# Kernel tuning notes

Hardware: AMD Instinct MI355X
Metric: run time of the kernel (lower is better)

## Reference

```python
import jax, jax.numpy as jnp
import numpy as np

N_NODES = 8192
N_EDGES = 262144
IN_DIM = 128
HID = 128
FLAT = N_NODES * HID  # 1048576


def gcn_conv(x, edge_index, W, b):
    """PyG-style GCNConv: add self-loops, symmetric deg^{-1/2} normalization,
    out[col] += norm * (x @ W)[row], plus bias."""
    N = x.shape[0]
    loop = jnp.arange(N)
    row = jnp.concatenate([edge_index[0], loop])  # source nodes
    col = jnp.concatenate([edge_index[1], loop])  # target nodes
    deg = jax.ops.segment_sum(jnp.ones_like(col, dtype=x.dtype), col, num_segments=N)
    dinv = jax.lax.rsqrt(jnp.maximum(deg, 1.0))  # deg >= 1 thanks to self-loops
    norm = dinv[row] * dinv[col]  # [E+N]
    h = x @ W  # [N, out]
    msg = h[row] * norm[:, None]  # gather
    out = jax.ops.segment_sum(msg, col, num_segments=N)  # scatter-add
    return out + b


def setup_inputs() -> dict:
    key = jax.random.key(0)
    ks = jax.random.split(key, 12)
    def lin(k, fan_in, shape):
        bound = 1.0 / np.sqrt(fan_in)
        return jax.random.uniform(k, shape, jnp.float32, -bound, bound)
    return {
        "x": jax.random.normal(ks[0], (N_NODES, IN_DIM), jnp.float32),
        "edge_index": jax.random.randint(ks[1], (2, N_EDGES), 0, N_NODES, jnp.int64 if jax.config.jax_enable_x64 else jnp.int32),
        "W1": lin(ks[2], IN_DIM, (IN_DIM, HID)),
        "b1": lin(ks[3], IN_DIM, (HID,)),
        "W2": lin(ks[4], HID, (HID, HID)),
        "b2": lin(ks[5], HID, (HID,)),
        "fc1_w": lin(ks[6], FLAT, (FLAT, HID)),
        "fc1_b": lin(ks[7], FLAT, (HID,)),
        "fc2_w": lin(ks[8], HID, (HID, HID)),
        "fc2_b": lin(ks[9], HID, (HID,)),
        "fc3_w": lin(ks[10], HID, (HID, 1)),
        "fc3_b": lin(ks[11], HID, (1,)),
    }


def reference(x, edge_index, W1, b1, W2, b2, fc1_w, fc1_b, fc2_w, fc2_b, fc3_w, fc3_b):
    e = jax.nn.relu(gcn_conv(x, edge_index, W1, b1))
    e = gcn_conv(e, edge_index, W2, b2)
    flat = e.reshape(-1)  # [N_NODES*HID]
    h = jax.nn.relu(flat @ fc1_w + fc1_b)
    h = jax.nn.relu(h @ fc2_w + fc2_b)
    q = h @ fc3_w + fc3_b  # [1]
    return q
```

## Files before the change

### kernel.cpp

```cpp
#include <hip/hip_runtime.h>

#define N_NODES 8192
#define N_EDGES 262144
#define DIM 128
#define NREP 64

typedef float fv4 __attribute__((ext_vector_type(4)));

__global__ void k_deg(const int* __restrict__ col, int* __restrict__ deg) {
    int e = blockIdx.x * blockDim.x + threadIdx.x;
    if (e < N_EDGES) atomicAdd(&deg[col[e]], 1);
}

__global__ __launch_bounds__(1024) void k_scan(const int* __restrict__ deg,
                                               int* __restrict__ rowptr,
                                               float* __restrict__ dinv) {
    __shared__ int wsum[16];
    __shared__ int wpre[16];
    int t = threadIdx.x;
    int base = t * 8;
    int v[8];
    int s = 0;
    #pragma unroll
    for (int i = 0; i < 8; ++i) {
        int d = deg[base + i];
        dinv[base + i] = rsqrtf((float)d + 1.0f);
        v[i] = s; s += d;
    }
    int lane = t & 63, wv = t >> 6;
    int incl = s;
    #pragma unroll
    for (int off = 1; off < 64; off <<= 1) {
        int n = __shfl_up(incl, off);
        if (lane >= off) incl += n;
    }
    if (lane == 63) wsum[wv] = incl;
    __syncthreads();
    if (t == 0) {
        int a = 0;
        #pragma unroll
        for (int i = 0; i < 16; ++i) { wpre[i] = a; a += wsum[i]; }
        rowptr[8192] = a;
    }
    __syncthreads();
    int ebase = wpre[wv] + incl - s;
    #pragma unroll
    for (int i = 0; i < 8; ++i) rowptr[base + i] = ebase + v[i];
}

__global__ void k_fill(const int* __restrict__ rows, const int* __restrict__ cols,
                       const int* __restrict__ rowptr, int* __restrict__ cnt,
                       int* __restrict__ srcs) {
    int e = blockIdx.x * blockDim.x + threadIdx.x;
    if (e < N_EDGES) {
        int c = cols[e];
        int p = atomicAdd(&cnt[c], 1);
        srcs[rowptr[c] + p] = rows[e];
    }
}

__global__ __launch_bounds__(256) void k_gemm(const float* __restrict__ x,
                                              const float* __restrict__ W,
                                              const float* __restrict__ dinv,
                                              float* __restrict__ out) {
    __shared__ float4 Wl[128 * 32];
    int t = threadIdx.x;
    const float4* W4 = (const float4*)W;
    for (int i = t; i < 128 * 32; i += 256) Wl[i] = W4[i];
    __syncthreads();

    int q  = t & 31;
    int rg = t >> 5;
    int row0 = blockIdx.x * 32;
    for (int p = 0; p < 4; ++p) {
        int row = row0 + p * 8 + rg;
        const float4* xr = (const float4*)(x + (size_t)row * DIM);
        float4 acc = {0.f, 0.f, 0.f, 0.f};
        #pragma unroll
        for (int k4 = 0; k4 < 32; ++k4) {
            float4 xv = xr[k4];
            float4 w0 = Wl[(k4 * 4 + 0) * 32 + q];
            float4 w1 = Wl[(k4 * 4 + 1) * 32 + q];
            float4 w2 = Wl[(k4 * 4 + 2) * 32 + q];
            float4 w3 = Wl[(k4 * 4 + 3) * 32 + q];
            acc.x += xv.x * w0.x + xv.y * w1.x + xv.z * w2.x + xv.w * w3.x;
            acc.y += xv.x * w0.y + xv.y * w1.y + xv.z * w2.y + xv.w * w3.y;
            acc.z += xv.x * w0.z + xv.y * w1.z + xv.z * w2.z + xv.w * w3.z;
            acc.w += xv.x * w0.w + xv.y * w1.w + xv.z * w2.w + xv.w * w3.w;
        }
        float s = dinv[row];
        acc.x *= s; acc.y *= s; acc.z *= s; acc.w *= s;
        ((float4*)(out + (size_t)row * DIM))[q] = acc;
    }
}

__device__ __forceinline__ float2 gather_row(const float2* __restrict__ H,
                                             const int* __restrict__ srcs,
                                             int beg, int end, int node, int lane) {
    float2 a0 = H[(size_t)node * 64 + lane];
    float2 a1 = {0.f, 0.f};
    int j = beg;
    int npre = (4 - (beg & 3)) & 3;
    if (npre > end - beg) npre = end - beg;
    for (int p = 0; p < npre; ++p, ++j) {
        float2 v = H[(size_t)srcs[j] * 64 + lane];
        a0.x += v.x; a0.y += v.y;
    }
    for (; j + 3 < end; j += 4) {
        int4 s4 = *reinterpret_cast<const int4*>(srcs + j);
        float2 v0 = H[(size_t)s4.x * 64 + lane];
        float2 v1 = H[(size_t)s4.y * 64 + lane];
        float2 v2 = H[(size_t)s4.z * 64 + lane];
        float2 v3 = H[(size_t)s4.w * 64 + lane];
        a0.x += v0.x + v2.x; a0.y += v0.y + v2.y;
        a1.x += v1.x + v3.x; a1.y += v1.y + v3.y;
    }
    for (; j < end; ++j) {
        float2 v = H[(size_t)srcs[j] * 64 + lane];
        a1.x += v.x; a1.y += v.y;
    }
    a0.x += a1.x; a0.y += a1.y;
    return a0;
}

__global__ __launch_bounds__(256) void k_gather(const float* __restrict__ h,
                                                const int* __restrict__ srcs,
                                                const int* __restrict__ rowptr,
                                                const float* __restrict__ dinv,
                                                const float* __restrict__ b,
                                                float* __restrict__ out) {
    int t = threadIdx.x;
    int lane = t & 63;
    int node = blockIdx.x * 4 + (t >> 6);
    float2 acc = gather_row((const float2*)h, srcs, rowptr[node], rowptr[node + 1], node, lane);
    float s = dinv[node];
    float2 bv = ((const float2*)b)[lane];
    float2 o;
    o.x = fmaxf(s * acc.x + bv.x, 0.f);
    o.y = fmaxf(s * acc.y + bv.y, 0.f);
    ((float2*)(out + (size_t)node * DIM))[lane] = o;
}

__global__ __launch_bounds__(256) void k_gfc(const float* __restrict__ h,
                                             const int* __restrict__ srcs,
                                             const int* __restrict__ rowptr,
                                             const float* __restrict__ dinv,
                                             const float* __restrict__ b,
                                             const float* __restrict__ w,
                                             float* __restrict__ facc_r) {
    __shared__ float oL[4][128];
    __shared__ fv4 red4[4][32];
    int t = threadIdx.x;
    int lane = t & 63;
    int wid = t >> 6;
    int node = blockIdx.x * 4 + wid;
    float2 acc = gather_row((const float2*)h, srcs, rowptr[node], rowptr[node + 1], node, lane);
    float s = dinv[node];
    float2 bv = ((const float2*)b)[lane];
    float2 o = { s * acc.x + bv.x, s * acc.y + bv.y };
    ((float2*)oL[wid])[lane] = o;
    __syncthreads();

    int q  = lane & 31;
    int kh = lane >> 5;
    size_t rowbase = (size_t)node * 128;
    fv4 a4 = {0.f, 0.f, 0.f, 0.f};
    #pragma unroll 8
    for (int k2 = 0; k2 < 64; ++k2) {
        int k = k2 * 2 + kh;
        float ok = oL[wid][k];
        const fv4* wp = (const fv4*)(w + (rowbase + k) * 128);
        fv4 wr = __builtin_nontemporal_load(wp + q);
        a4 += ok * wr;
    }
    a4.x += __shfl_xor(a4.x, 32);
    a4.y += __shfl_xor(a4.y, 32);
    a4.z += __shfl_xor(a4.z, 32);
    a4.w += __shfl_xor(a4.w, 32);
    if (lane < 32) red4[wid][q] = a4;
    __syncthreads();
    if (t < 128) {
        const float* rf = (const float*)red4;
        float val = (rf[t] + rf[128 + t]) + (rf[256 + t] + rf[384 + t]);
        atomicAdd(&facc_r[((blockIdx.x & (NREP - 1)) << 7) + t], val);
    }
}

__global__ __launch_bounds__(128) void k_tail(const float* __restrict__ facc_r,
                                              const float* __restrict__ fc1_b,
                                              const float* __restrict__ fc2_w,
                                              const float* __restrict__ fc2_b,
                                              const float* __restrict__ fc3_w,
                                              const float* __restrict__ fc3_b,
                                              float* __restrict__ out) {
    __shared__ float h1[128], red[128];
    int j = threadIdx.x;
    float a0 = 0.f;
    #pragma unroll
    for (int r = 0; r < NREP; ++r) a0 += facc_r[r * 128 + j];
    h1[j] = fmaxf(a0 + fc1_b[j], 0.f);
    __syncthreads();
    float a = 0.f;
    #pragma unroll 8
    for (int k = 0; k < 128; ++k) a += h1[k] * fc2_w[k * 128 + j];
    float h2 = fmaxf(a + fc2_b[j], 0.f);
    red[j] = h2 * fc3_w[j];
    __syncthreads();
    if (j == 0) {
        float s = 0.f;
        for (int k = 0; k < 128; ++k) s += red[k];
        out[0] = s + fc3_b[0];
    }
}

extern "C" void kernel_launch(void* const* d_in, const int* in_sizes, int n_in,
                              void* d_out, int out_size, void* d_ws, size_t ws_size,
                              hipStream_t stream) {
    const float* x     = (const float*)d_in[0];
    const int*   ei    = (const int*)d_in[1];
    const float* W1    = (const float*)d_in[2];
    const float* b1    = (const float*)d_in[3];
    const float* W2    = (const float*)d_in[4];
    const float* b2    = (const float*)d_in[5];
    const float* fc1_w = (const float*)d_in[6];
    const float* fc1_b = (const float*)d_in[7];
    const float* fc2_w = (const float*)d_in[8];
    const float* fc2_b = (const float*)d_in[9];
    const float* fc3_w = (const float*)d_in[10];
    const float* fc3_b = (const float*)d_in[11];
    const int* rows = ei;
    const int* cols = ei + N_EDGES;

    float* buf0   = (float*)d_ws;
    float* buf1   = buf0 + (size_t)N_NODES * DIM;
    int*   degi   = (int*)(buf1 + (size_t)N_NODES * DIM);
    int*   cnt    = degi + N_NODES;
    float* facc_r = (float*)(cnt + N_NODES);
    float* dinv   = facc_r + NREP * DIM;
    int*   rowptr = (int*)(dinv + N_NODES);
    int*   srcs   = rowptr + N_NODES + 8;
    float* out    = (float*)d_out;

    hipMemsetAsync(degi, 0, (2 * N_NODES) * sizeof(int) + NREP * DIM * sizeof(float), stream);

    k_deg<<<N_EDGES / 256, 256, 0, stream>>>(cols, degi);
    k_scan<<<1, 1024, 0, stream>>>(degi, rowptr, dinv);
    k_fill<<<N_EDGES / 256, 256, 0, stream>>>(rows, cols, rowptr, cnt, srcs);

    k_gemm<<<N_NODES / 32, 256, 0, stream>>>(x, W1, dinv, buf0);
    k_gather<<<N_NODES / 4, 256, 0, stream>>>(buf0, srcs, rowptr, dinv, b1, buf1);

    k_gemm<<<N_NODES / 32, 256, 0, stream>>>(buf1, W2, dinv, buf0);
    k_gfc<<<N_NODES / 4, 256, 0, stream>>>(buf0, srcs, rowptr, dinv, b2, fc1_w, facc_r);

    k_tail<<<1, 128, 0, stream>>>(facc_r, fc1_b, fc2_w, fc2_b, fc3_w, fc3_b, out);
}
```

Measured before the change: 838.9 us.

## Vectorize edge gather to float4 with half-wave edge split and trim syncs

The neighbor gather now has each lane load float4 columns. The two 32-lane halves of a wave take alternating edges, and the halves are combined with cross-lane shuffles, replacing the float2-per-lane gather. The block-wide barrier before the fc1 stage in k_gfc is removed, since each wave only reads its own shared row. The tail reduction uses wave shuffles instead of a serial loop, and the node GEMM processes 16 rows per block instead of 32 to launch more blocks. The aim is wider memory transactions and less synchronization, at the cost of extra shuffles and half-idle lanes in the final writes.

```diff
diff --git a/kernel.cpp b/kernel.cpp
--- a/kernel.cpp
+++ b/kernel.cpp
@@ -71,8 +71,8 @@
 
     int q  = t & 31;
     int rg = t >> 5;
-    int row0 = blockIdx.x * 32;
-    for (int p = 0; p < 4; ++p) {
+    int row0 = blockIdx.x * 16;
+    for (int p = 0; p < 2; ++p) {
         int row = row0 + p * 8 + rg;
         const float4* xr = (const float4*)(x + (size_t)row * DIM);
         float4 acc = {0.f, 0.f, 0.f, 0.f};
@@ -94,32 +94,32 @@
     }
 }
 
-__device__ __forceinline__ float2 gather_row(const float2* __restrict__ H,
-                                             const int* __restrict__ srcs,
-                                             int beg, int end, int node, int lane) {
-    float2 a0 = H[(size_t)node * 64 + lane];
-    float2 a1 = {0.f, 0.f};
+__device__ __forceinline__ fv4 gather_row4(const fv4* __restrict__ H4,
+                                           const int* __restrict__ srcs,
+                                           int beg, int end, int node,
+                                           int q, int half) {
+    fv4 a0 = {0.f, 0.f, 0.f, 0.f};
+    fv4 a1 = {0.f, 0.f, 0.f, 0.f};
+    if (!half) a0 = H4[(size_t)node * 32 + q];
     int j = beg;
-    int npre = (4 - (beg & 3)) & 3;
-    if (npre > end - beg) npre = end - beg;
-    for (int p = 0; p < npre; ++p, ++j) {
-        float2 v = H[(size_t)srcs[j] * 64 + lane];
-        a0.x += v.x; a0.y += v.y;
-    }
     for (; j + 3 < end; j += 4) {
-        int4 s4 = *reinterpret_cast<const int4*>(srcs + j);
-        float2 v0 = H[(size_t)s4.x * 64 + lane];
-        float2 v1 = H[(size_t)s4.y * 64 + lane];
-        float2 v2 = H[(size_t)s4.z * 64 + lane];
-        float2 v3 = H[(size_t)s4.w * 64 + lane];
-        a0.x += v0.x + v2.x; a0.y += v0.y + v2.y;
-        a1.x += v1.x + v3.x; a1.y += v1.y + v3.y;
-    }
-    for (; j < end; ++j) {
-        float2 v = H[(size_t)srcs[j] * 64 + lane];
-        a1.x += v.x; a1.y += v.y;
-    }
-    a0.x += a1.x; a0.y += a1.y;
+        int ra = srcs[j + half];
+        int rb = srcs[j + 2 + half];
+        a0 += H4[(size_t)ra * 32 + q];
+        a1 += H4[(size_t)rb * 32 + q];
+    }
+    for (; j + 1 < end; j += 2) {
+        int r = srcs[j + half];
+        a0 += H4[(size_t)r * 32 + q];
+    }
+    if (j < end && !half) {
+        a0 += H4[(size_t)srcs[j] * 32 + q];
+    }
+    a0 += a1;
+    a0.x += __shfl_xor(a0.x, 32);
+    a0.y += __shfl_xor(a0.y, 32);
+    a0.z += __shfl_xor(a0.z, 32);
+    a0.w += __shfl_xor(a0.w, 32);
     return a0;
 }
 
@@ -131,14 +131,17 @@
                                                 float* __restrict__ out) {
     int t = threadIdx.x;
     int lane = t & 63;
+    int q = lane & 31, half = lane >> 5;
     int node = blockIdx.x * 4 + (t >> 6);
-    float2 acc = gather_row((const float2*)h, srcs, rowptr[node], rowptr[node + 1], node, lane);
+    fv4 acc = gather_row4((const fv4*)h, srcs, rowptr[node], rowptr[node + 1], node, q, half);
     float s = dinv[node];
-    float2 bv = ((const float2*)b)[lane];
-    float2 o;
+    fv4 bv = ((const fv4*)b)[q];
+    fv4 o;
     o.x = fmaxf(s * acc.x + bv.x, 0.f);
     o.y = fmaxf(s * acc.y + bv.y, 0.f);
-    ((float2*)(out + (size_t)node * DIM))[lane] = o;
+    o.z = fmaxf(s * acc.z + bv.z, 0.f);
+    o.w = fmaxf(s * acc.w + bv.w, 0.f);
+    if (half == 0) ((fv4*)(out + (size_t)node * DIM))[q] = o;
 }
 
 __global__ __launch_bounds__(256) void k_gfc(const float* __restrict__ h,
@@ -153,16 +156,17 @@
     int t = threadIdx.x;
     int lane = t & 63;
     int wid = t >> 6;
+    int q = lane & 31, kh = lane >> 5;
     int node = blockIdx.x * 4 + wid;
-    float2 acc = gather_row((const float2*)h, srcs, rowptr[node], rowptr[node + 1], node, lane);
+    fv4 acc = gather_row4((const fv4*)h, srcs, rowptr[node], rowptr[node + 1], node, q, kh);
     float s = dinv[node];
-    float2 bv = ((const float2*)b)[lane];
-    float2 o = { s * acc.x + bv.x, s * acc.y + bv.y };
-    ((float2*)oL[wid])[lane] = o;
-    __syncthreads();
-
-    int q  = lane & 31;
-    int kh = lane >> 5;
+    fv4 bv = ((const fv4*)b)[q];
+    if (kh == 0) {
+        fv4 o = { s * acc.x + bv.x, s * acc.y + bv.y,
+                  s * acc.z + bv.z, s * acc.w + bv.w };
+        ((fv4*)oL[wid])[q] = o;
+    }
+
     size_t rowbase = (size_t)node * 128;
     fv4 a4 = {0.f, 0.f, 0.f, 0.f};
     #pragma unroll 8
@@ -206,10 +210,11 @@
     float h2 = fmaxf(a + fc2_b[j], 0.f);
     red[j] = h2 * fc3_w[j];
     __syncthreads();
-    if (j == 0) {
-        float s = 0.f;
-        for (int k = 0; k < 128; ++k) s += red[k];
-        out[0] = s + fc3_b[0];
+    if (j < 64) {
+        float v = red[j] + red[j + 64];
+        #pragma unroll
+        for (int off = 32; off; off >>= 1) v += __shfl_down(v, off);
+        if (j == 0) out[0] = v + fc3_b[0];
     }
 }
 
@@ -247,10 +252,10 @@
     k_scan<<<1, 1024, 0, stream>>>(degi, rowptr, dinv);
     k_fill<<<N_EDGES / 256, 256, 0, stream>>>(rows, cols, rowptr, cnt, srcs);
 
-    k_gemm<<<N_NODES / 32, 256, 0, stream>>>(x, W1, dinv, buf0);
+    k_gemm<<<N_NODES / 16, 256, 0, stream>>>(x, W1, dinv, buf0);
     k_gather<<<N_NODES / 4, 256, 0, stream>>>(buf0, srcs, rowptr, dinv, b1, buf1);
 
-    k_gemm<<<N_NODES / 32, 256, 0, stream>>>(buf1, W2, dinv, buf0);
+    k_gemm<<<N_NODES / 16, 256, 0, stream>>>(buf1, W2, dinv, buf0);
     k_gfc<<<N_NODES / 4, 256, 0, stream>>>(buf0, srcs, rowptr, dinv, b2, fc1_w, facc_r);
 
     k_tail<<<1, 128, 0, stream>>>(facc_r, fc1_b, fc2_w, fc2_b, fc3_w, fc3_b, out);
```

After: 856.8 us. 2.1% more time.
